# Performance work log

Hardware: AMD Instinct MI355X
Metric: run time of the kernel (lower is better)

Reference implementation:

```python
import jax, jax.numpy as jnp
import numpy as np

N = 50000
E = 800000
D = 16            # input_dim == hidden_dim == output_dim (required for consistency)
D2 = D * D
HEADS = 4
NEG_SLOPE = 0.2


def _gat_conv(x, src, dst, W, att_src, att_dst, bias):
    """PyG GATConv with concat=False (mean over heads), add_self_loops already applied.
    x: [N, Cin], W: [Cin, H*C], att_*: [H, C], bias: [C]."""
    H, C = att_src.shape
    xh = (x @ W).reshape(N, H, C)                     # [N, H, C]
    a_src = jnp.einsum('nhc,hc->nh', xh, att_src)      # [N, H]
    a_dst = jnp.einsum('nhc,hc->nh', xh, att_dst)
    alpha = jax.nn.leaky_relu(a_src[src] + a_dst[dst], NEG_SLOPE)   # [E, H]
    amax = jax.ops.segment_max(alpha, dst, num_segments=N)
    amax = jnp.where(jnp.isfinite(amax), amax, 0.0)
    ex = jnp.exp(alpha - jax.lax.stop_gradient(amax)[dst])
    denom = jax.ops.segment_sum(ex, dst, num_segments=N)
    coef = ex / (denom[dst] + 1e-16)                  # per-dst softmax over incoming edges
    acc = jnp.zeros((N, C), x.dtype)
    for h in range(H):  # loop over heads to avoid [E, H, C] intermediate
        acc = acc + jax.ops.segment_sum(coef[:, h:h + 1] * xh[src, h], dst, num_segments=N)
    return acc / H + bias


def setup_inputs() -> dict:
    key = jax.random.key(0)
    ks = jax.random.split(key, 20)
    s = lambda k, shape, fan: jax.random.normal(k, shape, jnp.float32) * (1.0 / np.sqrt(fan))
    inp = {
        'mean': jax.random.normal(ks[0], (N, D), jnp.float32),
        'cov': jax.random.normal(ks[1], (N, D, D), jnp.float32),
        'edge_index': jax.random.randint(ks[2], (2, E), 0, N, jnp.int32),
        # gat_mean params
        'W_mean': s(ks[3], (D, HEADS * D), D),
        'att_src_mean': s(ks[4], (HEADS, D), D),
        'att_dst_mean': s(ks[5], (HEADS, D), D),
        'bias_mean': jnp.zeros((D,), jnp.float32),
        # gat_cov params
        'W_cov': s(ks[6], (D2, HEADS * D2), D2),
        'att_src_cov': s(ks[7], (HEADS, D2), D2),
        'att_dst_cov': s(ks[8], (HEADS, D2), D2),
        'bias_cov': jnp.zeros((D2,), jnp.float32),
        # fc_mean: Linear(D,D) -> Linear(D,D)
        'fm_W1': s(ks[9], (D, D), D), 'fm_b1': jnp.zeros((D,), jnp.float32),
        'fm_W2': s(ks[10], (D, D), D), 'fm_b2': jnp.zeros((D,), jnp.float32),
        # fc_cov: Linear(D2,D2) -> Linear(D2,D2)
        'fcv_W1': s(ks[11], (D2, D2), D2), 'fcv_b1': jnp.zeros((D2,), jnp.float32),
        'fcv_W2': s(ks[12], (D2, D2), D2), 'fcv_b2': jnp.zeros((D2,), jnp.float32),
    }
    return inp


def reference(mean, cov, edge_index, W_mean, att_src_mean, att_dst_mean, bias_mean,
              W_cov, att_src_cov, att_dst_cov, bias_cov,
              fm_W1, fm_b1, fm_W2, fm_b2, fcv_W1, fcv_b1, fcv_W2, fcv_b2):
    loops = jnp.arange(N, dtype=edge_index.dtype)
    src = jnp.concatenate([edge_index[0], loops])
    dst = jnp.concatenate([edge_index[1], loops])

    cov_flat = cov.reshape(N, D2)
    mean_agg = _gat_conv(mean, src, dst, W_mean, att_src_mean, att_dst_mean, bias_mean)
    cov_agg = _gat_conv(cov_flat, src, dst, W_cov, att_src_cov, att_dst_cov, bias_cov)

    mean_out = (mean_agg @ fm_W1 + fm_b1) @ fm_W2 + fm_b2
    cov_out = (cov_agg @ fcv_W1 + fcv_b1) @ fcv_W2 + fcv_b2
    return mean_out, cov_out.reshape(N, D, D)
```

## Files before the change

### kernel.cpp

```cpp
#include <hip/hip_runtime.h>

#define NN 50000
#define EE 800000
#define DD 16
#define DD2 256
#define CAP 64

typedef __bf16 bf16x8 __attribute__((ext_vector_type(8)));
typedef float f32x4 __attribute__((ext_vector_type(4)));
typedef float f32x2 __attribute__((ext_vector_type(2)));

__device__ inline unsigned short f2bf(float f) {
    unsigned int u = __float_as_uint(f);
    return (unsigned short)((u + 0x7FFFu + ((u >> 16) & 1u)) >> 16);
}

__device__ inline void gl2lds16(const void* g, void* l) {
    __builtin_amdgcn_global_load_lds((const __attribute__((address_space(1))) unsigned int*)g,
                                     (__attribute__((address_space(3))) unsigned int*)l, 16, 0, 0);
}

__global__ void k_scatter(const int* ei, int* cursor, int* srt) {
    int i = blockIdx.x * 256 + threadIdx.x;
    if (i * 2 >= EE) return;
    int2 s2 = *(const int2*)(ei + i * 2);
    int2 d2 = *(const int2*)(ei + EE + i * 2);
    int p0 = atomicAdd(&cursor[d2.x], 1);
    if (p0 < CAP) srt[((size_t)d2.x << 6) + p0] = s2.x;
    int p1 = atomicAdd(&cursor[d2.y], 1);
    if (p1 < CAP) srt[((size_t)d2.y << 6) + p1] = s2.y;
}

__global__ void k_pre(const float* fcv_W1, const float* fcv_W2, const float* fcv_b1, const float* fcv_b2,
                      const float* fm_W1, const float* fm_W2, const float* fm_b1, const float* fm_b2,
                      const float* W_cov, const float* as_cov, const float* ad_cov,
                      const float* W_mean, const float* as_mean, const float* ad_mean,
                      const float* bias_cov, const float* bias_mean,
                      unsigned short* WpT, float* bpc, float* vcov, float* vmean,
                      float* Wpm, float* bpm) {
    __shared__ float sh[256];
    int b = blockIdx.x, t = threadIdx.x;
    if (b < 1024) {
        int q = b >> 8, i = b & 255;
        const float* wrow = W_cov + (size_t)i * 1024 + q * 256;
        float t1 = 0.f;
        for (int j = 0; j < 256; ++j) t1 += wrow[j] * fcv_W1[j * 256 + t];
        sh[t] = t1;
        __syncthreads();
        float s = 0.f;
        for (int k = 0; k < 256; ++k) s += sh[k] * fcv_W2[k * 256 + t];
        int C = q * 32 + (i >> 3);
        int cs = C ^ (t & 7);
        WpT[(size_t)t * 1024 + cs * 8 + (i & 7)] = f2bf(0.25f * s);
    } else if (b == 1024) {
        float t1 = fcv_b1[t];
        for (int j = 0; j < 256; ++j) t1 += bias_cov[j] * fcv_W1[j * 256 + t];
        sh[t] = t1;
        __syncthreads();
        float s = fcv_b2[t];
        for (int k = 0; k < 256; ++k) s += sh[k] * fcv_W2[k * 256 + t];
        bpc[t] = s;
    } else if (b < 1033) {
        int ch = b - 1025, h = ch & 3;
        const float* att = (ch < 4) ? as_cov : ad_cov;
        int jl = t & 31, i8 = t >> 5;
        float av[8];
#pragma unroll
        for (int jj = 0; jj < 8; ++jj) av[jj] = att[h * 256 + jj * 32 + jl];
        for (int ii = 0; ii < 32; ++ii) {
            int i = ii * 8 + i8;
            const float* wr = W_cov + (size_t)i * 1024 + h * 256;
            float p = 0.f;
#pragma unroll
            for (int jj = 0; jj < 8; ++jj) p += wr[jj * 32 + jl] * av[jj];
#pragma unroll
            for (int off = 16; off; off >>= 1) p += __shfl_xor(p, off);
            if (jl == 0) vcov[ch * 256 + i] = p;
        }
    } else {
        {
            int j = t >> 4, c = t & 15;
            float s = 0.f;
            for (int k = 0; k < 16; ++k) s += fm_W1[j * 16 + k] * fm_W2[k * 16 + c];
            sh[j * 16 + c] = s;
        }
        if (t < 128) {
            int ch = t >> 4, i = t & 15, h = ch & 3;
            const float* att = (ch < 4) ? as_mean : ad_mean;
            float s = 0.f;
            for (int j = 0; j < 16; ++j) s += W_mean[i * 64 + h * 16 + j] * att[h * 16 + j];
            vmean[ch * 16 + i] = s;
        }
        __syncthreads();
#pragma unroll
        for (int r = 0; r < 4; ++r) {
            int idx = r * 256 + t;
            int k = idx >> 4, c = idx & 15, h = k >> 4, i = k & 15;
            float s = 0.f;
            for (int j = 0; j < 16; ++j) s += W_mean[i * 64 + h * 16 + j] * sh[j * 16 + c];
            Wpm[k * 16 + c] = 0.25f * s;
        }
        if (t < 16) {
            float b2 = fm_b2[t];
            for (int k = 0; k < 16; ++k) b2 += fm_b1[k] * fm_W2[k * 16 + t];
            float s = b2;
            for (int j = 0; j < 16; ++j) s += bias_mean[j] * sh[j * 16 + t];
            bpm[t] = s;
        }
    }
}

__global__ void __launch_bounds__(256) k_dots(const float* cov, const float* mean,
                                              const float* vcov, const float* vmean,
                                              float* asrc, float* adst, unsigned short* covb,
                                              int* cursor, int* srt) {
    __shared__ float vcs[8 * 256];
    __shared__ float vms[128];
    __shared__ float xrow[4][256];
    int t = threadIdx.x;
#pragma unroll
    for (int r = 0; r < 2; ++r) {
        int i = r * 256 + t;
        int k4 = i >> 6, l = i & 63;
        *(float4*)&vcs[i * 4] = *(const float4*)&vcov[(l >> 3) * 256 + (l & 7) * 32 + k4 * 4];
    }
    if (t < 128) vms[t] = vmean[t];
    int w = t >> 6, lane = t & 63;
    int n = blockIdx.x * 4 + w;
    int c = lane >> 3, g = lane & 7;
    if (lane == 0) {
        cursor[n] = 1;
        srt[(size_t)n << 6] = n;
    }
    float4 x = *(const float4*)(cov + (size_t)n * 256 + lane * 4);
    unsigned int u0 = (unsigned int)f2bf(x.x) | ((unsigned int)f2bf(x.y) << 16);
    unsigned int u1 = (unsigned int)f2bf(x.z) | ((unsigned int)f2bf(x.w) << 16);
    *(uint2*)((char*)covb + (size_t)n * 512 + lane * 8) = make_uint2(u0, u1);
    *(float4*)&xrow[w][((lane & 7) * 8 + (lane >> 3)) * 4] = x;
    __syncthreads();
    float p = 0.f;
#pragma unroll
    for (int k4 = 0; k4 < 8; ++k4) {
        float4 xv = *(const float4*)&xrow[w][(k4 * 8 + g) * 4];
        float4 vv = *(const float4*)&vcs[k4 * 256 + lane * 4];
        p += xv.x * vv.x + xv.y * vv.y + xv.z * vv.z + xv.w * vv.w;
    }
    float m0 = mean[(size_t)n * 16 + g * 2];
    float m1 = mean[(size_t)n * 16 + g * 2 + 1];
    float q = m0 * vms[c * 16 + g * 2] + m1 * vms[c * 16 + g * 2 + 1];
#pragma unroll
    for (int off = 1; off <= 4; off <<= 1) {
        p += __shfl_xor(p, off);
        q += __shfl_xor(q, off);
    }
    if (g == 0) {
        if (c < 4) {
            asrc[(size_t)n * 8 + c] = p;
            asrc[(size_t)n * 8 + 4 + c] = q;
        } else {
            adst[(size_t)n * 8 + (c - 4)] = p;
            adst[(size_t)n * 8 + 4 + (c - 4)] = q;
        }
    }
}

__global__ void __launch_bounds__(256, 8) k_agg(const int* __restrict__ cnt, const int* __restrict__ srt,
                                                const float* __restrict__ asrc, const float* __restrict__ adst,
                                                const unsigned short* __restrict__ covb, const float* __restrict__ mean,
                                                unsigned short* __restrict__ Ycat, float* __restrict__ Ym) {
    __shared__ float exbuf[4][64][8];
    __shared__ float mrow[4][64][16];
    int t = threadIdx.x;
    int w = t >> 6, lane = t & 63;
    int ml = lane & 15;
    int hl4 = lane >> 4;
    const char* covbc = (const char*)covb;
    const char* meanc = (const char*)mean;
    const char* asrcc = (const char*)asrc;
    unsigned lodc = (unsigned)lane << 3;
    float* exw = &exbuf[w][0][0];
    float* mrw = &mrow[w][0][0];

    for (int n0 = blockIdx.x * 4; n0 < NN; n0 += gridDim.x * 4) {
        int nu = __builtin_amdgcn_readfirstlane(n0 + w);
        int beg = nu << 6;
        int deg = min(cnt[nu], CAP);

        f32x2 acc[8];
#pragma unroll
        for (int k = 0; k < 8; ++k) acc[k] = (f32x2){0.f, 0.f};
        float accm = 0.f;
        float dsc[4] = {0, 0, 0, 0};
        float dsm = 0.f;

        auto loadg = [&](int jp, int s0v, uint2* cd) {
#pragma unroll
            for (int k2 = 0; k2 < 4; ++k2) {
                int se = __shfl(s0v, jp + k2);
                cd[k2] = *(const uint2*)(covbc + (((unsigned)se << 9) + lodc));
            }
        };
        auto compute4 = [&](int jp, const uint2* cd) {
#pragma unroll
            for (int k2 = 0; k2 < 4; ++k2) {
                int e = jp + k2;
                float4 e0 = *(const float4*)(exw + e * 8);
                float em = exw[e * 8 + 4 + hl4];
                float mv = mrw[e * 16 + (ml ^ ((e & 7) << 1))];
                f32x2 x0 = (f32x2){__uint_as_float(cd[k2].x << 16), __uint_as_float(cd[k2].x & 0xffff0000u)};
                f32x2 x1 = (f32x2){__uint_as_float(cd[k2].y << 16), __uint_as_float(cd[k2].y & 0xffff0000u)};
                float ev[4] = {e0.x, e0.y, e0.z, e0.w};
#pragma unroll
                for (int h = 0; h < 4; ++h) {
                    f32x2 e2 = (f32x2){ev[h], ev[h]};
                    acc[h * 2 + 0] = __builtin_elementwise_fma(e2, x0, acc[h * 2 + 0]);
                    acc[h * 2 + 1] = __builtin_elementwise_fma(e2, x1, acc[h * 2 + 1]);
                }
                dsc[0] += e0.x; dsc[1] += e0.y; dsc[2] += e0.z; dsc[3] += e0.w;
                accm += em * mv;
                dsm += em;
            }
        };

        {
            bool valid = lane < deg;
            int s0 = srt[beg + (valid ? lane : (deg - 1))];
            int cnt8 = (deg + 7) & ~7;

            uint2 cdA[4], cdB[4];
            loadg(0, s0, cdA);
            loadg(4, s0, cdB);

            {
                const float4* pm = (const float4*)(meanc + ((size_t)((unsigned)s0 << 6)));
                bool oddE = lane & 1;
                int g0 = (lane >> 1) & 3;
                float* mb = mrw + lane * 16;
                float4 F0 = pm[0], F1 = pm[1];
                float4 V0 = oddE ? make_float4(F0.z, F0.w, F0.x, F0.y) : F0;
                float4 V1 = oddE ? make_float4(F1.z, F1.w, F1.x, F1.y) : F1;
                *(float4*)(mb + ((0 ^ g0) << 2)) = V0;
                *(float4*)(mb + ((1 ^ g0) << 2)) = V1;
                float4 F2 = pm[2], F3 = pm[3];
                float4 V2 = oddE ? make_float4(F2.z, F2.w, F2.x, F2.y) : F2;
                float4 V3 = oddE ? make_float4(F3.z, F3.w, F3.x, F3.y) : F3;
                *(float4*)(mb + ((2 ^ g0) << 2)) = V2;
                *(float4*)(mb + ((3 ^ g0) << 2)) = V3;
            }

            {
                const float4* pa = (const float4*)(asrcc + ((size_t)((unsigned)s0 << 5)));
                float4 a0 = pa[0], a1 = pa[1];
                const float4* pd = (const float4*)(adst + (size_t)nu * 8);
                float4 d0 = pd[0], d1 = pd[1];
                float av[8] = {a0.x, a0.y, a0.z, a0.w, a1.x, a1.y, a1.z, a1.w};
                float ad[8] = {d0.x, d0.y, d0.z, d0.w, d1.x, d1.y, d1.z, d1.w};
                float ex8[8];
#pragma unroll
                for (int c = 0; c < 8; ++c) {
                    float al = av[c] + ad[c];
                    al = (al >= 0.f) ? al : 0.2f * al;
                    float e = __expf(al);
                    ex8[c] = valid ? e : 0.f;
                }
                *(float4*)(exw + lane * 8) = make_float4(ex8[0], ex8[1], ex8[2], ex8[3]);
                *(float4*)(exw + lane * 8 + 4) = make_float4(ex8[4], ex8[5], ex8[6], ex8[7]);
            }

            for (int jp = 0; jp < cnt8; jp += 8) {
                compute4(jp, cdA);
                if (jp + 8 < cnt8) loadg(jp + 8, s0, cdA);
                compute4(jp + 4, cdB);
                if (jp + 12 < cnt8) loadg(jp + 12, s0, cdB);
            }
        }

        float invc[4] = {1.f / (dsc[0] + 1e-16f), 1.f / (dsc[1] + 1e-16f),
                         1.f / (dsc[2] + 1e-16f), 1.f / (dsc[3] + 1e-16f)};
        float invm = 1.f / (dsm + 1e-16f);
        char* yrow = (char*)Ycat + (size_t)nu * 2048;
        int cbase = lane >> 1, hl = lane & 1, sw = nu & 7;
#pragma unroll
        for (int h = 0; h < 4; ++h) {
            float iv = invc[h];
            uint2 pk;
            pk.x = (unsigned int)f2bf(acc[h * 2 + 0].x * iv) | ((unsigned int)f2bf(acc[h * 2 + 0].y * iv) << 16);
            pk.y = (unsigned int)f2bf(acc[h * 2 + 1].x * iv) | ((unsigned int)f2bf(acc[h * 2 + 1].y * iv) << 16);
            int cs = (h * 32 + cbase) ^ sw;
            *(uint2*)(yrow + cs * 16 + hl * 8) = pk;
        }
        Ym[(size_t)nu * 64 + lane] = accm * invm;
    }
}

__global__ void __launch_bounds__(256) k_gemm(const unsigned short* Ycat, const unsigned short* WpT,
                                              const float* bpc, float* out_cov,
                                              const float* Ym, const float* Wpm, const float* bpm,
                                              float* out_mean) {
    __shared__ __align__(16) unsigned short As[2][128 * 64];
    __shared__ __align__(16) unsigned short Bs[2][128 * 64];
    int t = threadIdx.x;
    if (blockIdx.x >= 782) {
        float* wm = (float*)As[0];
        float* bmv = (float*)Bs[0];
        for (int i = t; i < 1024; i += 256) wm[i] = Wpm[i];
        if (t < 16) bmv[t] = bpm[t];
        __syncthreads();
        int base = (blockIdx.x - 782) * 256;
        int c = t & 15;
#pragma unroll
        for (int p = 0; p < 16; ++p) {
            int node = base + p * 16 + (t >> 4);
            if (node < NN) {
                const float* yr = Ym + (size_t)node * 64;
                float s = bmv[c];
#pragma unroll
                for (int k = 0; k < 64; ++k) s += yr[k] * wm[k * 16 + c];
                out_mean[(size_t)node * 16 + c] = s;
            }
        }
        return;
    }
    int m0 = (blockIdx.x >> 1) * 128, c0 = (blockIdx.x & 1) * 128;
    int w = t >> 6, lane = t & 63;
    int mg = w >> 1, ng = w & 1;
    int q = lane >> 4, lm = lane & 15;
    f32x4 acc[4][4];
#pragma unroll
    for (int mt = 0; mt < 4; ++mt)
#pragma unroll
        for (int nt = 0; nt < 4; ++nt) acc[mt][nt] = (f32x4){0.f, 0.f, 0.f, 0.f};

    auto stage = [&](int kc, int buf) {
        int k0 = kc * 64;
#pragma unroll
        for (int i2 = 0; i2 < 4; ++i2) {
            int idx = t + i2 * 256;
            int row = idx >> 3, seg = idx & 7;
            int gm = m0 + row;
            if (gm > NN - 1) gm = NN - 1;
            gl2lds16(Ycat + (size_t)gm * 1024 + k0 + seg * 8, As[buf] + idx * 8);
        }
#pragma unroll
        for (int i2 = 0; i2 < 4; ++i2) {
            int idx = t + i2 * 256;
            int col = idx >> 3, seg = idx & 7;
            gl2lds16(WpT + (size_t)(c0 + col) * 1024 + k0 + seg * 8, Bs[buf] + idx * 8);
        }
    };

    stage(0, 0);
    int cur = 0;
    for (int kc = 0; kc < 16; ++kc) {
        if (kc < 15) {
            stage(kc + 1, cur ^ 1);
            asm volatile("s_waitcnt vmcnt(8)" ::: "memory");
        } else {
            asm volatile("s_waitcnt vmcnt(0)" ::: "memory");
        }
        __builtin_amdgcn_s_barrier();
        const unsigned short* Ab = As[cur];
        const unsigned short* Bb = Bs[cur];
#pragma unroll
        for (int ks = 0; ks < 2; ++ks) {
            bf16x8 af[4], bfr[4];
#pragma unroll
            for (int mt = 0; mt < 4; ++mt) {
                int row = mg * 64 + mt * 16 + lm;
                int ch = (ks * 4 + q) ^ (row & 7);
                af[mt] = *(const bf16x8*)(Ab + row * 64 + ch * 8);
            }
#pragma unroll
            for (int nt = 0; nt < 4; ++nt) {
                int col = ng * 64 + nt * 16 + lm;
                int ch = (ks * 4 + q) ^ (col & 7);
                bfr[nt] = *(const bf16x8*)(Bb + col * 64 + ch * 8);
            }
#pragma unroll
            for (int mt = 0; mt < 4; ++mt)
#pragma unroll
                for (int nt = 0; nt < 4; ++nt)
                    acc[mt][nt] = __builtin_amdgcn_mfma_f32_16x16x32_bf16(af[mt], bfr[nt], acc[mt][nt], 0, 0, 0);
        }
        __builtin_amdgcn_s_barrier();
        cur ^= 1;
    }
#pragma unroll
    for (int nt = 0; nt < 4; ++nt) {
        int col = c0 + ng * 64 + nt * 16 + lm;
        float bias = bpc[col];
#pragma unroll
        for (int mt = 0; mt < 4; ++mt) {
#pragma unroll
            for (int e = 0; e < 4; ++e) {
                int r = m0 + mg * 64 + mt * 16 + q * 4 + e;
                if (r < NN)
                    __builtin_nontemporal_store(acc[mt][nt][e] + bias, &out_cov[(size_t)r * 256 + col]);
            }
        }
    }
}

extern "C" void kernel_launch(void* const* d_in, const int* in_sizes, int n_in,
                              void* d_out, int out_size, void* d_ws, size_t ws_size,
                              hipStream_t stream) {
    const float* mean = (const float*)d_in[0];
    const float* cov = (const float*)d_in[1];
    const int* ei = (const int*)d_in[2];
    const float* W_mean = (const float*)d_in[3];
    const float* as_mean = (const float*)d_in[4];
    const float* ad_mean = (const float*)d_in[5];
    const float* bias_mean = (const float*)d_in[6];
    const float* W_cov = (const float*)d_in[7];
    const float* as_cov = (const float*)d_in[8];
    const float* ad_cov = (const float*)d_in[9];
    const float* bias_cov = (const float*)d_in[10];
    const float* fm_W1 = (const float*)d_in[11];
    const float* fm_b1 = (const float*)d_in[12];
    const float* fm_W2 = (const float*)d_in[13];
    const float* fm_b2 = (const float*)d_in[14];
    const float* fcv_W1 = (const float*)d_in[15];
    const float* fcv_b1 = (const float*)d_in[16];
    const float* fcv_W2 = (const float*)d_in[17];
    const float* fcv_b2 = (const float*)d_in[18];

    float* out_mean = (float*)d_out;
    float* out_cov = (float*)d_out + (size_t)NN * DD;

    char* w = (char*)d_ws;
    auto alloc = [&](size_t bytes) -> void* {
        void* p = (void*)w;
        w += (bytes + 255) & ~(size_t)255;
        return p;
    };
    unsigned short* Ycat = (unsigned short*)alloc((size_t)NN * 1024 * 2);
    unsigned short* covb = (unsigned short*)alloc((size_t)NN * 256 * 2);
    float* Ym = (float*)alloc((size_t)NN * 64 * 4);
    int* cursor = (int*)alloc(NN * 4);
    int* srt = (int*)alloc((size_t)NN * CAP * 4);
    float* asrc = (float*)alloc((size_t)NN * 8 * 4);
    float* adst = (float*)alloc((size_t)NN * 8 * 4);
    float* vcov = (float*)alloc(8 * 256 * 4);
    float* vmean = (float*)alloc(8 * 16 * 4);
    unsigned short* WpT = (unsigned short*)alloc(256 * 1024 * 2);
    float* bpc = (float*)alloc(256 * 4);
    float* Wpm = (float*)alloc(64 * 16 * 4);
    float* bpm = (float*)alloc(16 * 4);

    k_pre<<<1034, 256, 0, stream>>>(fcv_W1, fcv_W2, fcv_b1, fcv_b2, fm_W1, fm_W2, fm_b1, fm_b2,
                                    W_cov, as_cov, ad_cov, W_mean, as_mean, ad_mean,
                                    bias_cov, bias_mean, WpT, bpc, vcov, vmean, Wpm, bpm);
    k_dots<<<NN / 4, 256, 0, stream>>>(cov, mean, vcov, vmean, asrc, adst, covb, cursor, srt);
    k_scatter<<<(EE / 2 + 255) / 256, 256, 0, stream>>>(ei, cursor, srt);
    k_agg<<<1536, 256, 0, stream>>>(cursor, srt, asrc, adst, covb, mean, Ycat, Ym);
    k_gemm<<<782 + 196, 256, 0, stream>>>(Ycat, WpT, bpc, out_cov, Ym, Wpm, bpm, out_mean);
}
```

Baseline: 389.4 us.

## Fuse edge scatter into weight precompute kernel and synthesize self-loops in aggregation

The edge-bucketing scatter moves into the weight-precompute launch as extra blocks, so both independent jobs can run at the same time and one launch is dropped. Self-loops are no longer written into the bucket arrays by the dots kernel. The aggregation kernel now appends the node itself as an implicit last neighbor, and a memset clears the cursor array. Capacity for real edges drops to CAP-1, and a partial unroll pragma is added to the precompute loops.

```diff
diff --git a/kernel.cpp b/kernel.cpp
--- a/kernel.cpp
+++ b/kernel.cpp
@@ -20,44 +20,49 @@
                                      (__attribute__((address_space(3))) unsigned int*)l, 16, 0, 0);
 }
 
-__global__ void k_scatter(const int* ei, int* cursor, int* srt) {
-    int i = blockIdx.x * 256 + threadIdx.x;
-    if (i * 2 >= EE) return;
-    int2 s2 = *(const int2*)(ei + i * 2);
-    int2 d2 = *(const int2*)(ei + EE + i * 2);
-    int p0 = atomicAdd(&cursor[d2.x], 1);
-    if (p0 < CAP) srt[((size_t)d2.x << 6) + p0] = s2.x;
-    int p1 = atomicAdd(&cursor[d2.y], 1);
-    if (p1 < CAP) srt[((size_t)d2.y << 6) + p1] = s2.y;
-}
-
-__global__ void k_pre(const float* fcv_W1, const float* fcv_W2, const float* fcv_b1, const float* fcv_b2,
-                      const float* fm_W1, const float* fm_W2, const float* fm_b1, const float* fm_b2,
-                      const float* W_cov, const float* as_cov, const float* ad_cov,
-                      const float* W_mean, const float* as_mean, const float* ad_mean,
-                      const float* bias_cov, const float* bias_mean,
-                      unsigned short* WpT, float* bpc, float* vcov, float* vmean,
-                      float* Wpm, float* bpm) {
+__global__ void k_scat_pre(const float* fcv_W1, const float* fcv_W2, const float* fcv_b1, const float* fcv_b2,
+                           const float* fm_W1, const float* fm_W2, const float* fm_b1, const float* fm_b2,
+                           const float* W_cov, const float* as_cov, const float* ad_cov,
+                           const float* W_mean, const float* as_mean, const float* ad_mean,
+                           const float* bias_cov, const float* bias_mean,
+                           unsigned short* WpT, float* bpc, float* vcov, float* vmean,
+                           float* Wpm, float* bpm,
+                           const int* ei, int* cursor, int* srt) {
     __shared__ float sh[256];
     int b = blockIdx.x, t = threadIdx.x;
+    if (b >= 1034) {
+        int i = (b - 1034) * 256 + t;
+        if (i * 2 >= EE) return;
+        int2 s2 = *(const int2*)(ei + i * 2);
+        int2 d2 = *(const int2*)(ei + EE + i * 2);
+        int p0 = atomicAdd(&cursor[d2.x], 1);
+        if (p0 < CAP) srt[((size_t)d2.x << 6) + p0] = s2.x;
+        int p1 = atomicAdd(&cursor[d2.y], 1);
+        if (p1 < CAP) srt[((size_t)d2.y << 6) + p1] = s2.y;
+        return;
+    }
     if (b < 1024) {
         int q = b >> 8, i = b & 255;
         const float* wrow = W_cov + (size_t)i * 1024 + q * 256;
         float t1 = 0.f;
+#pragma unroll 4
         for (int j = 0; j < 256; ++j) t1 += wrow[j] * fcv_W1[j * 256 + t];
         sh[t] = t1;
         __syncthreads();
         float s = 0.f;
+#pragma unroll 4
         for (int k = 0; k < 256; ++k) s += sh[k] * fcv_W2[k * 256 + t];
         int C = q * 32 + (i >> 3);
         int cs = C ^ (t & 7);
         WpT[(size_t)t * 1024 + cs * 8 + (i & 7)] = f2bf(0.25f * s);
     } else if (b == 1024) {
         float t1 = fcv_b1[t];
+#pragma unroll 4
         for (int j = 0; j < 256; ++j) t1 += bias_cov[j] * fcv_W1[j * 256 + t];
         sh[t] = t1;
         __syncthreads();
         float s = fcv_b2[t];
+#pragma unroll 4
         for (int k = 0; k < 256; ++k) s += sh[k] * fcv_W2[k * 256 + t];
         bpc[t] = s;
     } else if (b < 1033) {
@@ -112,8 +117,7 @@
 
 __global__ void __launch_bounds__(256) k_dots(const float* cov, const float* mean,
                                               const float* vcov, const float* vmean,
-                                              float* asrc, float* adst, unsigned short* covb,
-                                              int* cursor, int* srt) {
+                                              float* asrc, float* adst, unsigned short* covb) {
     __shared__ float vcs[8 * 256];
     __shared__ float vms[128];
     __shared__ float xrow[4][256];
@@ -128,10 +132,6 @@
     int w = t >> 6, lane = t & 63;
     int n = blockIdx.x * 4 + w;
     int c = lane >> 3, g = lane & 7;
-    if (lane == 0) {
-        cursor[n] = 1;
-        srt[(size_t)n << 6] = n;
-    }
     float4 x = *(const float4*)(cov + (size_t)n * 256 + lane * 4);
     unsigned int u0 = (unsigned int)f2bf(x.x) | ((unsigned int)f2bf(x.y) << 16);
     unsigned int u1 = (unsigned int)f2bf(x.z) | ((unsigned int)f2bf(x.w) << 16);
@@ -184,7 +184,7 @@
     for (int n0 = blockIdx.x * 4; n0 < NN; n0 += gridDim.x * 4) {
         int nu = __builtin_amdgcn_readfirstlane(n0 + w);
         int beg = nu << 6;
-        int deg = min(cnt[nu], CAP);
+        int deg = min(cnt[nu], CAP - 1);
 
         f32x2 acc[8];
 #pragma unroll
@@ -223,9 +223,9 @@
         };
 
         {
-            bool valid = lane < deg;
-            int s0 = srt[beg + (valid ? lane : (deg - 1))];
-            int cnt8 = (deg + 7) & ~7;
+            bool valid = lane <= deg;
+            int s0 = (lane < deg) ? srt[beg + lane] : nu;
+            int cnt8 = (deg + 1 + 7) & ~7;
 
             uint2 cdA[4], cdB[4];
             loadg(0, s0, cdA);
@@ -447,11 +447,12 @@
     float* Wpm = (float*)alloc(64 * 16 * 4);
     float* bpm = (float*)alloc(16 * 4);
 
-    k_pre<<<1034, 256, 0, stream>>>(fcv_W1, fcv_W2, fcv_b1, fcv_b2, fm_W1, fm_W2, fm_b1, fm_b2,
-                                    W_cov, as_cov, ad_cov, W_mean, as_mean, ad_mean,
-                                    bias_cov, bias_mean, WpT, bpc, vcov, vmean, Wpm, bpm);
-    k_dots<<<NN / 4, 256, 0, stream>>>(cov, mean, vcov, vmean, asrc, adst, covb, cursor, srt);
-    k_scatter<<<(EE / 2 + 255) / 256, 256, 0, stream>>>(ei, cursor, srt);
+    hipMemsetAsync(cursor, 0, NN * 4, stream);
+    k_scat_pre<<<1034 + 1563, 256, 0, stream>>>(fcv_W1, fcv_W2, fcv_b1, fcv_b2, fm_W1, fm_W2, fm_b1, fm_b2,
+                                                W_cov, as_cov, ad_cov, W_mean, as_mean, ad_mean,
+                                                bias_cov, bias_mean, WpT, bpc, vcov, vmean, Wpm, bpm,
+                                                ei, cursor, srt);
+    k_dots<<<NN / 4, 256, 0, stream>>>(cov, mean, vcov, vmean, asrc, adst, covb);
     k_agg<<<1536, 256, 0, stream>>>(cursor, srt, asrc, adst, covb, mean, Ycat, Ym);
     k_gemm<<<782 + 196, 256, 0, stream>>>(Ycat, WpT, bpc, out_cov, Ym, Wpm, bpm, out_mean);
 }
```

Result: slower. 401.1 us (+3.0%).
